# Optimization experiments

Hardware: AMD Instinct MI355X
Metric: run time of the kernel (lower is better)

Reference implementation:

```python
import jax, jax.numpy as jnp
import numpy as np

N = 262144  # num_channels (o*i)
K = 5       # kernel_size


def setup_inputs() -> dict:
    key = jax.random.key(0)
    k1, k2, k3 = jax.random.split(key, 3)
    return {
        "input_filter": jax.random.normal(k1, (N, K, K, K), dtype=jnp.float32),
        "theta_v": jax.random.normal(k2, (N, 3), dtype=jnp.float32),
        "theta": jax.random.normal(k3, (N,), dtype=jnp.float32),
    }


def _rodrigues(theta_v, theta):
    # F.normalize(theta_v, p=2) with eps=1e-12
    norm = jnp.linalg.norm(theta_v, axis=-1, keepdims=True)
    v = theta_v / jnp.maximum(norm, 1e-12)
    vx, vy, vz = v[:, 0], v[:, 1], v[:, 2]
    z = jnp.zeros_like(vx)
    # skew-symmetric cross-product matrix m, shape (n,3,3)
    m = jnp.stack([z, -vz, vy,
                   vz, z, -vx,
                   -vy, vx, z], axis=-1).reshape(-1, 3, 3)
    s = jnp.sin(theta)[:, None, None]
    c = (1.0 - jnp.cos(theta))[:, None, None]
    I3 = jnp.eye(3, dtype=theta_v.dtype)
    return I3 + s * m + c * jnp.einsum('nij,njk->nik', m, m)


def _base_grid(k):
    # matches _get_base_grids: coord along axis i -> channel 0, j -> 1, l -> 2
    c = jnp.linspace(-1.0, 1.0, k, dtype=jnp.float32)
    gi, gj, gl = jnp.meshgrid(c, c, c, indexing='ij')
    return jnp.stack([gi, gj, gl], axis=-1).reshape(k * k * k, 3)  # (k^3, 3)


def _grid_sample_3d_zeros(vol, grid):
    # vol: (n, D, H, W); grid: (n, P, 3) in [-1,1], channels (x->W, y->H, z->D)
    # trilinear, align_corners=True, padding_mode='zeros'
    n, D, H, W = vol.shape
    x = (grid[..., 0] + 1.0) * 0.5 * (W - 1)
    y = (grid[..., 1] + 1.0) * 0.5 * (H - 1)
    z = (grid[..., 2] + 1.0) * 0.5 * (D - 1)
    x0f, y0f, z0f = jnp.floor(x), jnp.floor(y), jnp.floor(z)
    wx, wy, wz = x - x0f, y - y0f, z - z0f
    x0, y0, z0 = x0f.astype(jnp.int32), y0f.astype(jnp.int32), z0f.astype(jnp.int32)
    bidx = jnp.arange(n)[:, None]
    out = jnp.zeros(grid.shape[:-1], dtype=vol.dtype)
    for dz in (0, 1):
        for dy in (0, 1):
            for dx in (0, 1):
                zi, yi, xi = z0 + dz, y0 + dy, x0 + dx
                w = ((wz if dz else 1.0 - wz) *
                     (wy if dy else 1.0 - wy) *
                     (wx if dx else 1.0 - wx))
                inb = ((zi >= 0) & (zi < D) & (yi >= 0) & (yi < H) &
                       (xi >= 0) & (xi < W))
                v = vol[bidx,
                        jnp.clip(zi, 0, D - 1),
                        jnp.clip(yi, 0, H - 1),
                        jnp.clip(xi, 0, W - 1)]
                out = out + w * jnp.where(inb, v, jnp.zeros_like(v))
    return out


def reference(input_filter, theta_v, theta):
    n = theta_v.shape[0]
    k = input_filter.shape[-1]
    vol = input_filter.reshape(n, k, k, k)
    R = _rodrigues(theta_v, theta)                    # (n,3,3)
    base = _base_grid(k)                              # (k^3,3)
    grids = jnp.einsum('pj,njk->npk', base, R)        # (n,k^3,3) = base @ R
    out = _grid_sample_3d_zeros(vol, grids)           # (n,k^3)
    return out.reshape(input_filter.shape)
```

## Files before the change

kernel.cpp:

```cpp
#include <hip/hip_runtime.h>
#include <math.h>

#define KP    125
#define VOL7P 344
#define WPB   4
#define NF    8

typedef _Float16 half_t;
typedef half_t h2 __attribute__((ext_vector_type(2)));
typedef __fp16 fp16x2 __attribute__((ext_vector_type(2)));

static __device__ __forceinline__ h2 h2fma(h2 a, h2 b, h2 c) {
    return __builtin_elementwise_fma(a, b, c);
}
static __device__ __forceinline__ h2 cvt_pk(float a, float b) {
    fp16x2 t = __builtin_amdgcn_cvt_pkrtz(a, b);
    return __builtin_bit_cast(h2, t);
}
static __device__ __forceinline__ float rdlane(float v, int k) {
    return __builtin_bit_cast(float,
        __builtin_amdgcn_readlane(__builtin_bit_cast(int, v), k));
}

__global__ __launch_bounds__(WPB * 64) void fastrot_kernel(
    const float* __restrict__ vol,
    const float* __restrict__ theta_v,
    const float* __restrict__ theta,
    float* __restrict__ out)
{
    __shared__ __align__(16) unsigned int pad[WPB][VOL7P];

    const int lane = threadIdx.x & 63;
    const int ws   = __builtin_amdgcn_readfirstlane(threadIdx.x >> 6);
    const long long base = ((long long)blockIdx.x * WPB + ws) * NF;

    uint4* b0 = (uint4*)(&pad[ws][0]);
    const uint4 z4 = make_uint4(0u, 0u, 0u, 0u);
    b0[lane] = z4;
    if (lane < (VOL7P / 4 - 64)) b0[lane + 64] = z4;

    float r00, r01, r02, r10, r11, r12, r20, r21, r22;
    {
        const long long m = base + (lane & (NF - 1));
        const float ax = theta_v[m * 3 + 0];
        const float ay = theta_v[m * 3 + 1];
        const float az = theta_v[m * 3 + 2];
        const float th = theta[m];
        const float d2  = ax * ax + ay * ay + az * az;
        const float inv = rsqrtf(fmaxf(d2, 1e-24f));
        const float vx = ax * inv, vy = ay * inv, vz = az * inv;
        float s, cth;
        __sincosf(th, &s, &cth);
        const float c = 1.0f - cth;
        r00 = 1.0f - c * (vy * vy + vz * vz);
        r01 = -s * vz + c * (vx * vy);
        r02 =  s * vy + c * (vx * vz);
        r10 =  s * vz + c * (vx * vy);
        r11 = 1.0f - c * (vx * vx + vz * vz);
        r12 = -s * vx + c * (vy * vz);
        r20 = -s * vy + c * (vx * vz);
        r21 =  s * vx + c * (vy * vz);
        r22 = 1.0f - c * (vx * vx + vy * vy);
    }

    const int p0 = lane, p1 = lane + 64;
    const int i0 = (p0 * 41) >> 10;
    const int q0 = (p0 * 205) >> 10;
    const int j0 = q0 - i0 * 5;
    const int l0 = p0 - q0 * 5;
    const int i1 = (p1 * 41) >> 10;
    const int q1 = (p1 * 205) >> 10;
    const int j1 = q1 - i1 * 5;
    const int l1 = p1 - q1 * 5;
    const bool has1 = (p1 < KP);
    const int e0 = i0 * 49 + j0 * 7 + l0 + 57;
    const int e1 = i1 * 49 + j1 * 7 + l1 + 57;
    const float Bi0 = (float)(i0 - 2), Bj0 = (float)(j0 - 2), Bl0 = (float)(l0 - 2);
    const float Bi1 = (float)(i1 - 2), Bj1 = (float)(j1 - 2), Bl1 = (float)(l1 - 2);

    float fv0[NF], fv1[NF], nx0[NF], nx1[NF];
#pragma unroll
    for (int k = 0; k < NF; ++k) {
        const float* vn = vol + (base + k) * KP;
        fv0[k] = vn[p0];
        fv1[k] = has1 ? vn[p1] : 0.0f;
        nx0[k] = (l0 < 4) ? vn[p0 + 1] : 0.0f;
        nx1[k] = (has1 && l1 < 4) ? vn[p1 + 1] : 0.0f;
    }

    unsigned int* buf = &pad[ws][0];

#pragma unroll
    for (int k = 0; k < NF; ++k) {
        const float R00 = rdlane(r00, k), R01 = rdlane(r01, k), R02 = rdlane(r02, k);
        const float R10 = rdlane(r10, k), R11 = rdlane(r11, k), R12 = rdlane(r12, k);
        const float R20 = rdlane(r20, k), R21 = rdlane(r21, k), R22 = rdlane(r22, k);

        buf[e0] = __builtin_bit_cast(unsigned int, cvt_pk(fv0[k], nx0[k]));
        if (l0 == 0)
            buf[e0 - 1] = __builtin_bit_cast(unsigned int, cvt_pk(0.0f, fv0[k]));
        if (has1) {
            buf[e1] = __builtin_bit_cast(unsigned int, cvt_pk(fv1[k], nx1[k]));
            if (l1 == 0)
                buf[e1 - 1] = __builtin_bit_cast(unsigned int, cvt_pk(0.0f, fv1[k]));
        }

        float* on = out + (base + k) * KP;

        auto sample = [&](float Bi, float Bj, float Bl) -> float {
            float xf = fmaf(Bi, R00, fmaf(Bj, R10, fmaf(Bl, R20, 3.0f)));
            float yf = fmaf(Bi, R01, fmaf(Bj, R11, fmaf(Bl, R21, 3.0f)));
            float zf = fmaf(Bi, R02, fmaf(Bj, R12, fmaf(Bl, R22, 3.0f)));
            xf = fminf(fmaxf(xf, 0.0f), 5.99993896f);
            yf = fminf(fmaxf(yf, 0.0f), 5.99993896f);
            zf = fminf(fmaxf(zf, 0.0f), 5.99993896f);
            const int x0 = (int)xf, y0 = (int)yf, z0 = (int)zf;
            const float wx = __builtin_amdgcn_fractf(xf);
            const float wy = __builtin_amdgcn_fractf(yf);
            const float wz = __builtin_amdgcn_fractf(zf);
            const int ci = z0 * 49 + y0 * 7 + x0;

            const h2 A0 = __builtin_bit_cast(h2, buf[ci]);
            const h2 A1 = __builtin_bit_cast(h2, buf[ci + 49]);
            const h2 B0 = __builtin_bit_cast(h2, buf[ci + 7]);
            const h2 B1 = __builtin_bit_cast(h2, buf[ci + 56]);

            const h2 wzh = cvt_pk(wz, wz);
            const h2 wyh = cvt_pk(wy, wy);
            const h2 E = h2fma(wzh, A1 - A0, A0);
            const h2 F = h2fma(wzh, B1 - B0, B0);
            const h2 G = h2fma(wyh, F - E, E);
            const float g0 = (float)G.x;
            const float g1 = (float)G.y;
            return fmaf(wx, g1 - g0, g0);
        };

        on[p0] = sample(Bi0, Bj0, Bl0);
        if (has1) on[p1] = sample(Bi1, Bj1, Bl1);
    }
}

extern "C" void kernel_launch(void* const* d_in, const int* in_sizes, int n_in,
                              void* d_out, int out_size, void* d_ws, size_t ws_size,
                              hipStream_t stream) {
    const float* vol     = (const float*)d_in[0];
    const float* theta_v = (const float*)d_in[1];
    const float* theta   = (const float*)d_in[2];
    float* out           = (float*)d_out;

    const int N = in_sizes[2];

    fastrot_kernel<<<N / (WPB * NF), WPB * 64, 0, stream>>>(vol, theta_v, theta, out);
}
```

Measured before the change: 56.37 us.

## Exploit point symmetry of grid pairs and double-buffer LDS volume

Pairs each lane's point p with its mirror 124-p, so that point's rotated coordinate is derived as 6 minus the first one rather than recomputed. This removes the has1 predication and the extra index math, but lane 62 now handles the centre point twice with a redundant store. The per-warp LDS volume is also double-buffered across filters, so writes for the next filter do not overwrite data still being read. The cost is twice the LDS footprint, which may reduce occupancy.

New measurement: 52.70 us, median of 2. -6.5%, faster.

```diff
diff --git a/kernel.cpp b/kernel.cpp
--- a/kernel.cpp
+++ b/kernel.cpp
@@ -28,16 +28,18 @@
     const float* __restrict__ theta,
     float* __restrict__ out)
 {
-    __shared__ __align__(16) unsigned int pad[WPB][VOL7P];
+    __shared__ __align__(16) unsigned int pad[WPB][2][VOL7P];
 
     const int lane = threadIdx.x & 63;
     const int ws   = __builtin_amdgcn_readfirstlane(threadIdx.x >> 6);
     const long long base = ((long long)blockIdx.x * WPB + ws) * NF;
 
-    uint4* b0 = (uint4*)(&pad[ws][0]);
+    uint4* f0 = (uint4*)(&pad[ws][0][0]);
+    uint4* f1 = (uint4*)(&pad[ws][1][0]);
     const uint4 z4 = make_uint4(0u, 0u, 0u, 0u);
-    b0[lane] = z4;
-    if (lane < (VOL7P / 4 - 64)) b0[lane + 64] = z4;
+    f0[lane] = z4;
+    f1[lane] = z4;
+    if (lane < (VOL7P / 4 - 64)) { f0[lane + 64] = z4; f1[lane + 64] = z4; }
 
     float r00, r01, r02, r10, r11, r12, r20, r21, r22;
     {
@@ -63,35 +65,31 @@
         r22 = 1.0f - c * (vx * vx + vy * vy);
     }
 
-    const int p0 = lane, p1 = lane + 64;
+    const int p0 = lane;
+    const int p1 = 124 - lane;
     const int i0 = (p0 * 41) >> 10;
     const int q0 = (p0 * 205) >> 10;
     const int j0 = q0 - i0 * 5;
     const int l0 = p0 - q0 * 5;
-    const int i1 = (p1 * 41) >> 10;
-    const int q1 = (p1 * 205) >> 10;
-    const int j1 = q1 - i1 * 5;
-    const int l1 = p1 - q1 * 5;
-    const bool has1 = (p1 < KP);
+    const int i1 = 4 - i0, j1 = 4 - j0, l1 = 4 - l0;
     const int e0 = i0 * 49 + j0 * 7 + l0 + 57;
     const int e1 = i1 * 49 + j1 * 7 + l1 + 57;
     const float Bi0 = (float)(i0 - 2), Bj0 = (float)(j0 - 2), Bl0 = (float)(l0 - 2);
-    const float Bi1 = (float)(i1 - 2), Bj1 = (float)(j1 - 2), Bl1 = (float)(l1 - 2);
 
     float fv0[NF], fv1[NF], nx0[NF], nx1[NF];
 #pragma unroll
     for (int k = 0; k < NF; ++k) {
         const float* vn = vol + (base + k) * KP;
         fv0[k] = vn[p0];
-        fv1[k] = has1 ? vn[p1] : 0.0f;
+        fv1[k] = vn[p1];
         nx0[k] = (l0 < 4) ? vn[p0 + 1] : 0.0f;
-        nx1[k] = (has1 && l1 < 4) ? vn[p1 + 1] : 0.0f;
+        nx1[k] = (l1 < 4) ? vn[p1 + 1] : 0.0f;
     }
-
-    unsigned int* buf = &pad[ws][0];
 
 #pragma unroll
     for (int k = 0; k < NF; ++k) {
+        unsigned int* buf = &pad[ws][k & 1][0];
+
         const float R00 = rdlane(r00, k), R01 = rdlane(r01, k), R02 = rdlane(r02, k);
         const float R10 = rdlane(r10, k), R11 = rdlane(r11, k), R12 = rdlane(r12, k);
         const float R20 = rdlane(r20, k), R21 = rdlane(r21, k), R22 = rdlane(r22, k);
@@ -99,18 +97,17 @@
         buf[e0] = __builtin_bit_cast(unsigned int, cvt_pk(fv0[k], nx0[k]));
         if (l0 == 0)
             buf[e0 - 1] = __builtin_bit_cast(unsigned int, cvt_pk(0.0f, fv0[k]));
-        if (has1) {
-            buf[e1] = __builtin_bit_cast(unsigned int, cvt_pk(fv1[k], nx1[k]));
-            if (l1 == 0)
-                buf[e1 - 1] = __builtin_bit_cast(unsigned int, cvt_pk(0.0f, fv1[k]));
-        }
+        buf[e1] = __builtin_bit_cast(unsigned int, cvt_pk(fv1[k], nx1[k]));
+        if (l1 == 0)
+            buf[e1 - 1] = __builtin_bit_cast(unsigned int, cvt_pk(0.0f, fv1[k]));
 
         float* on = out + (base + k) * KP;
 
-        auto sample = [&](float Bi, float Bj, float Bl) -> float {
-            float xf = fmaf(Bi, R00, fmaf(Bj, R10, fmaf(Bl, R20, 3.0f)));
-            float yf = fmaf(Bi, R01, fmaf(Bj, R11, fmaf(Bl, R21, 3.0f)));
-            float zf = fmaf(Bi, R02, fmaf(Bj, R12, fmaf(Bl, R22, 3.0f)));
+        const float xr = fmaf(Bi0, R00, fmaf(Bj0, R10, fmaf(Bl0, R20, 3.0f)));
+        const float yr = fmaf(Bi0, R01, fmaf(Bj0, R11, fmaf(Bl0, R21, 3.0f)));
+        const float zr = fmaf(Bi0, R02, fmaf(Bj0, R12, fmaf(Bl0, R22, 3.0f)));
+
+        auto gather = [&](float xf, float yf, float zf) -> float {
             xf = fminf(fmaxf(xf, 0.0f), 5.99993896f);
             yf = fminf(fmaxf(yf, 0.0f), 5.99993896f);
             zf = fminf(fmaxf(zf, 0.0f), 5.99993896f);
@@ -135,8 +132,8 @@
             return fmaf(wx, g1 - g0, g0);
         };
 
-        on[p0] = sample(Bi0, Bj0, Bl0);
-        if (has1) on[p1] = sample(Bi1, Bj1, Bl1);
+        on[p0] = gather(xr, yr, zr);
+        on[p1] = gather(6.0f - xr, 6.0f - yr, 6.0f - zr);
     }
 }
 
```
